# Kernel tuning notes

Measured on AMD Instinct MI355X. Metric: run time of the kernel, lower is better.

## Reference

```python
import jax, jax.numpy as jnp
import numpy as np

BATCH, SEQ, D_MODEL = 2, 2048, 1024
NUM_HEADS = 16
D_K = D_MODEL // NUM_HEADS  # 64
ROPE_THETA = 10000.0


def setup_inputs() -> dict:
    key = jax.random.key(0)
    ks = jax.random.split(key, 5)
    sigma = np.sqrt(2.0 / (D_MODEL + D_MODEL))
    return {
        "x": jax.random.normal(ks[0], (BATCH, SEQ, D_MODEL), dtype=jnp.float32),
        "Wq": jax.random.normal(ks[1], (D_MODEL, D_MODEL), dtype=jnp.float32) * sigma,
        "Wk": jax.random.normal(ks[2], (D_MODEL, D_MODEL), dtype=jnp.float32) * sigma,
        "Wv": jax.random.normal(ks[3], (D_MODEL, D_MODEL), dtype=jnp.float32) * sigma,
        "Wo": jax.random.normal(ks[4], (D_MODEL, D_MODEL), dtype=jnp.float32) * sigma,
        "token_positions": jnp.arange(SEQ, dtype=jnp.int32),
    }


def _rope(t, cos, sin):
    # t: [b, h, s, d_k]; cos/sin: [s, d_k//2]
    even, odd = t[..., ::2], t[..., 1::2]
    out_even = even * cos - odd * sin
    out_odd = odd * cos + even * sin
    return jnp.stack([out_even, out_odd], axis=-1).reshape(t.shape)


def reference(x, Wq, Wk, Wv, Wo, token_positions):
    b, s, d = x.shape
    h, dk = NUM_HEADS, D_K

    def split_heads(w):
        # Linear: einsum('... d_in, d_out d_in -> ... d_out')
        y = jnp.einsum('bsd,ed->bse', x, w)
        return y.reshape(b, s, h, dk).transpose(0, 2, 1, 3)  # [b,h,s,dk]

    q, k, v = split_heads(Wq), split_heads(Wk), split_heads(Wv)

    # RoPE tables from token positions
    inv_freq = 1.0 / (ROPE_THETA ** (jnp.arange(0, dk, 2, dtype=jnp.float32) / dk))
    freqs = token_positions.astype(jnp.float32)[:, None] * inv_freq[None, :]  # [s, dk/2]
    cos, sin = jnp.cos(freqs), jnp.sin(freqs)
    q = _rope(q, cos, sin)
    k = _rope(k, cos, sin)

    scale = 1.0 / jnp.sqrt(jnp.asarray(dk, dtype=x.dtype))
    scores = jnp.einsum('bhqd,bhkd->bhqk', q, k) * scale  # [b,h,s,s]
    causal = jnp.tril(jnp.ones((s, s), dtype=bool))
    scores = jnp.where(causal, scores, -jnp.inf)
    probs = jax.nn.softmax(scores, axis=-1)
    out = jnp.einsum('bhqk,bhkd->bhqd', probs, v)
    out = out.transpose(0, 2, 1, 3).reshape(b, s, d)
    return jnp.einsum('bsd,ed->bse', out, Wo)
```

## Files before the change

kernel.cpp:

```cpp
#include <hip/hip_runtime.h>
#include <hip/hip_bf16.h>


#define BATCH   2
#define SEQLEN  2048
#define DMODEL  1024
#define NHEADS  16
#define DK      64

typedef __attribute__((ext_vector_type(8))) short bf16x8;
typedef __attribute__((ext_vector_type(4))) short bf16x4;
typedef __attribute__((ext_vector_type(4))) float f32x4;

__device__ __forceinline__ void gload_lds16(const void* g, void* l) {
  __builtin_amdgcn_global_load_lds(
      (const __attribute__((address_space(1))) unsigned int*)g,
      (__attribute__((address_space(3))) unsigned int*)l, 16, 0, 0);
}

__device__ __forceinline__ float fast_exp2(float x) {
#if __has_builtin(__builtin_amdgcn_exp2f)
  return __builtin_amdgcn_exp2f(x);
#else
  return exp2f(x);
#endif
}

__global__ __launch_bounds__(256) void cast_all(
    const float* __restrict__ x,  const float* __restrict__ wq,
    const float* __restrict__ wk, const float* __restrict__ wv,
    const float* __restrict__ wo,
    __hip_bfloat16* __restrict__ xb,  __hip_bfloat16* __restrict__ wqb,
    __hip_bfloat16* __restrict__ wkb, __hip_bfloat16* __restrict__ wvb,
    __hip_bfloat16* __restrict__ wob) {
  const size_t MM = (size_t)1 << 20;
  size_t i = ((size_t)blockIdx.x * 256 + threadIdx.x) * 8;
  const float* src; __hip_bfloat16* dst; size_t off = i;
  if (i < 4 * MM)      { src = x;  dst = xb; }
  else if (i < 5 * MM) { src = wq; dst = wqb; off = i - 4 * MM; }
  else if (i < 6 * MM) { src = wk; dst = wkb; off = i - 5 * MM; }
  else if (i < 7 * MM) { src = wv; dst = wvb; off = i - 6 * MM; }
  else                 { src = wo; dst = wob; off = i - 7 * MM; }
  float4 a = *(const float4*)(src + off);
  float4 b = *(const float4*)(src + off + 4);
  __hip_bfloat16 t[8];
  t[0] = __float2bfloat16(a.x); t[1] = __float2bfloat16(a.y);
  t[2] = __float2bfloat16(a.z); t[3] = __float2bfloat16(a.w);
  t[4] = __float2bfloat16(b.x); t[5] = __float2bfloat16(b.y);
  t[6] = __float2bfloat16(b.z); t[7] = __float2bfloat16(b.w);
  *(bf16x8*)(dst + off) = *(const bf16x8*)t;
}

__device__ __forceinline__ void gemm_core(
    const __hip_bfloat16* __restrict__ A, const __hip_bfloat16* __restrict__ W,
    int bm, int bn, int K, f32x4 (&acc)[4][4]) {
  __shared__ __hip_bfloat16 As[128 * 32];
  __shared__ __hip_bfloat16 Ws[128 * 32];
  const int tid  = threadIdx.x;
  const int wave = tid >> 6, lane = tid & 63;
  const int col  = lane & 15, quad = lane >> 4;
  const int wm   = (wave & 1) * 64, wn = (wave >> 1) * 64;
  const int srow = wave * 32;
  const int l4   = lane >> 2, sl = lane & 3;

  for (int k0 = 0; k0 < K; k0 += 32) {
#pragma unroll
    for (int c = 0; c < 2; ++c) {
      int r = srow + c * 16 + l4;
      int g = sl ^ (r & 3);
      gload_lds16(A + (size_t)(bm + r) * K + k0 + g * 8, &As[(srow + c * 16) * 32]);
      gload_lds16(W + (size_t)(bn + r) * K + k0 + g * 8, &Ws[(srow + c * 16) * 32]);
    }
    __syncthreads();
    bf16x8 af[4], bfr[4];
#pragma unroll
    for (int mt = 0; mt < 4; ++mt) {
      int r = wm + mt * 16 + col;
      af[mt] = *(const bf16x8*)&As[r * 32 + ((quad ^ (r & 3)) * 8)];
    }
#pragma unroll
    for (int nt = 0; nt < 4; ++nt) {
      int r = wn + nt * 16 + col;
      bfr[nt] = *(const bf16x8*)&Ws[r * 32 + ((quad ^ (r & 3)) * 8)];
    }
#pragma unroll
    for (int mt = 0; mt < 4; ++mt)
#pragma unroll
      for (int nt = 0; nt < 4; ++nt)
        acc[mt][nt] = __builtin_amdgcn_mfma_f32_16x16x32_bf16(af[mt], bfr[nt], acc[mt][nt], 0, 0, 0);
    __syncthreads();
  }
}

__global__ __launch_bounds__(256) void mfma_qkv(
    const __hip_bfloat16* __restrict__ xb,
    const __hip_bfloat16* __restrict__ wqb,
    const __hip_bfloat16* __restrict__ wkb,
    const __hip_bfloat16* __restrict__ wvb,
    __hip_bfloat16* __restrict__ Qw,
    __hip_bfloat16* __restrict__ Kw,
    __hip_bfloat16* __restrict__ Vtw) {
  const int z = blockIdx.z;
  const __hip_bfloat16* W = (z == 0) ? wqb : (z == 1) ? wkb : wvb;
  const int bm = blockIdx.x * 128, bn = blockIdx.y * 128;
  f32x4 acc[4][4] = {};
  gemm_core(xb, W, bm, bn, DMODEL, acc);

  const int wave = threadIdx.x >> 6, lane = threadIdx.x & 63;
  const int col  = lane & 15, quad = lane >> 4;
  const int wm   = (wave & 1) * 64, wn = (wave >> 1) * 64;

  if (z < 2) {
    __hip_bfloat16* C = (z == 0) ? Qw : Kw;
#pragma unroll
    for (int mt = 0; mt < 4; ++mt)
#pragma unroll
      for (int nt = 0; nt < 4; ++nt) {
        int n = bn + wn + nt * 16 + col;
#pragma unroll
        for (int r = 0; r < 4; ++r) {
          int m = bm + wm + mt * 16 + quad * 4 + r;
          C[(size_t)m * DMODEL + n] = __float2bfloat16(acc[mt][nt][r]);
        }
      }
  } else {
#pragma unroll
    for (int mt = 0; mt < 4; ++mt)
#pragma unroll
      for (int nt = 0; nt < 4; ++nt) {
        int n  = bn + wn + nt * 16 + col;
        int m0 = bm + wm + mt * 16 + quad * 4;
        __hip_bfloat16 t[4];
#pragma unroll
        for (int r = 0; r < 4; ++r) t[r] = __float2bfloat16(acc[mt][nt][r]);
        size_t off = (((size_t)(m0 >> 11) * NHEADS + (n >> 6)) * DK + (n & 63)) * SEQLEN + (m0 & 2047);
        *(bf16x4*)(Vtw + off) = *(const bf16x4*)t;
      }
  }
}

__global__ __launch_bounds__(256) void mfma_out(
    const __hip_bfloat16* __restrict__ Ow,
    const __hip_bfloat16* __restrict__ wob,
    float* __restrict__ out) {
  const int bm = blockIdx.x * 128, bn = blockIdx.y * 128;
  f32x4 acc[4][4] = {};
  gemm_core(Ow, wob, bm, bn, DMODEL, acc);
  const int wave = threadIdx.x >> 6, lane = threadIdx.x & 63;
  const int col  = lane & 15, quad = lane >> 4;
  const int wm   = (wave & 1) * 64, wn = (wave >> 1) * 64;
#pragma unroll
  for (int mt = 0; mt < 4; ++mt)
#pragma unroll
    for (int nt = 0; nt < 4; ++nt) {
      int n = bn + wn + nt * 16 + col;
#pragma unroll
      for (int r = 0; r < 4; ++r) {
        int m = bm + wm + mt * 16 + quad * 4 + r;
        out[(size_t)m * DMODEL + n] = acc[mt][nt][r];
      }
    }
}

__global__ __launch_bounds__(256) void rope_kernel(
    __hip_bfloat16* __restrict__ Q,
    __hip_bfloat16* __restrict__ Kt,
    const int* __restrict__ pos, int npairs) {
  int idx = blockIdx.x * blockDim.x + threadIdx.x;
  if (idx >= npairs) return;
  int ip = idx & 511;
  int s  = (idx >> 9) & (SEQLEN - 1);
  int p  = ip & 31;
  float inv_freq = exp2f(-13.287712379549449f * ((float)(2 * p) / 64.0f));
  float ang = (float)pos[s] * inv_freq;
  float sn, cs;
  sincosf(ang, &sn, &cs);
  const float SCL = 0.18033688011112042f;
  size_t off = (size_t)idx * 2;
  float qe = __bfloat162float(Q[off]), qo = __bfloat162float(Q[off + 1]);
  Q[off]     = __float2bfloat16((qe * cs - qo * sn) * SCL);
  Q[off + 1] = __float2bfloat16((qo * cs + qe * sn) * SCL);
  float ke = __bfloat162float(Kt[off]), ko = __bfloat162float(Kt[off + 1]);
  Kt[off]     = __float2bfloat16(ke * cs - ko * sn);
  Kt[off + 1] = __float2bfloat16(ko * cs + ke * sn);
}

__global__ __launch_bounds__(256) void attn_mfma(
    const __hip_bfloat16* __restrict__ Q,
    const __hip_bfloat16* __restrict__ K,
    const __hip_bfloat16* __restrict__ Vt,
    __hip_bfloat16* __restrict__ O) {
  __shared__ __align__(16) __hip_bfloat16 Ks[2][64 * 64];
  __shared__ __align__(16) __hip_bfloat16 Vs[2][64 * 64];
  __shared__ __align__(16) __hip_bfloat16 Pl[4][16 * 64];
  const int bh = blockIdx.y;
  const int b = bh >> 4, h = bh & 15;
  const int strip = 31 - (int)blockIdx.x;
  const int wave = threadIdx.x >> 6;
  const int lane = threadIdx.x & 63;
  const int col = lane & 15;
  const int quad = lane >> 4;
  const int q0 = strip * 64 + wave * 16;
  const int cswz = col & 7;

  const size_t qkbase = ((size_t)b * SEQLEN) * DMODEL + (size_t)h * DK;
  const size_t vbase  = (size_t)bh * DK * SEQLEN;
  __hip_bfloat16* pl = &Pl[wave][0];

  const int srow = lane >> 3;
  const int slot = lane & 7;

  auto stage = [&](int t, int buf) {
    const int j0 = t * 64;
#pragma unroll
    for (int c = 0; c < 2; ++c) {
      const int r = wave * 16 + c * 8 + srow;
      const int g = slot ^ (r & 7);
      gload_lds16(K + qkbase + (size_t)(j0 + r) * DMODEL + g * 8,
                  &Ks[buf][(wave * 16 + c * 8) * 64]);
      gload_lds16(Vt + vbase + (size_t)r * SEQLEN + j0 + g * 8,
                  &Vs[buf][(wave * 16 + c * 8) * 64]);
    }
  };

  bf16x8 qf[2];
#pragma unroll
  for (int kc = 0; kc < 2; ++kc)
    qf[kc] = *(const bf16x8*)(Q + qkbase + (size_t)(q0 + col) * DMODEL + kc * 32 + quad * 8);

  f32x4 acc[4] = {};
  float m_i = -1e30f, l_i = 0.f;
  const int ntiles = strip + 1;

  stage(0, 0);
  __syncthreads();

  for (int t = 0; t < ntiles; ++t) {
    const int buf = t & 1;
    if (t + 1 < ntiles) stage(t + 1, buf ^ 1);
    const int j0 = t * 64;

    f32x4 s[4] = {};
#pragma unroll
    for (int kt = 0; kt < 4; ++kt) {
      const int row = kt * 16 + col;
#pragma unroll
      for (int kc = 0; kc < 2; ++kc) {
        bf16x8 kf = *(const bf16x8*)&Ks[buf][row * 64 + (((kc * 4 + quad) ^ cswz) * 8)];
        s[kt] = __builtin_amdgcn_mfma_f32_16x16x32_bf16(kf, qf[kc], s[kt], 0, 0, 0);
      }
    }

    if (t == strip) {
      const int q = q0 + col;
#pragma unroll
      for (int kt = 0; kt < 4; ++kt)
#pragma unroll
        for (int r = 0; r < 4; ++r)
          if (j0 + kt * 16 + quad * 4 + r > q) s[kt][r] = -1e30f;
    }

    float mx = m_i;
#pragma unroll
    for (int kt = 0; kt < 4; ++kt)
#pragma unroll
      for (int r = 0; r < 4; ++r) mx = fmaxf(mx, s[kt][r]);
    mx = fmaxf(mx, __shfl_xor(mx, 16, 64));
    mx = fmaxf(mx, __shfl_xor(mx, 32, 64));
    float alpha = fast_exp2(m_i - mx);
    m_i = mx;

    float rs = 0.f;
#pragma unroll
    for (int kt = 0; kt < 4; ++kt) {
      __hip_bfloat16 tp[4];
#pragma unroll
      for (int r = 0; r < 4; ++r) {
        float pv = fast_exp2(s[kt][r] - mx);
        rs += pv;
        tp[r] = __float2bfloat16(pv);
      }
      int c = ((kt << 1) | (quad >> 1)) ^ cswz;
      *(bf16x4*)(pl + col * 64 + c * 8 + (quad & 1) * 4) = *(const bf16x4*)tp;
    }
    rs += __shfl_xor(rs, 16, 64);
    rs += __shfl_xor(rs, 32, 64);
    l_i = l_i * alpha + rs;
#pragma unroll
    for (int dt = 0; dt < 4; ++dt) acc[dt] *= alpha;

#pragma unroll
    for (int jc = 0; jc < 2; ++jc) {
      int c = ((jc << 2) | quad) ^ cswz;
      bf16x8 pf = *(const bf16x8*)(pl + col * 64 + c * 8);
#pragma unroll
      for (int dt = 0; dt < 4; ++dt) {
        const int dv = dt * 16 + col;
        bf16x8 vf = *(const bf16x8*)&Vs[buf][dv * 64 + (((jc * 4 + quad) ^ cswz) * 8)];
        acc[dt] = __builtin_amdgcn_mfma_f32_16x16x32_bf16(vf, pf, acc[dt], 0, 0, 0);
      }
    }

    __syncthreads();
  }

  const float inv = 1.f / l_i;
  const size_t orow = qkbase + (size_t)(q0 + col) * DMODEL;
#pragma unroll
  for (int dt = 0; dt < 4; ++dt) {
    __hip_bfloat16 tp[4];
#pragma unroll
    for (int r = 0; r < 4; ++r) tp[r] = __float2bfloat16(acc[dt][r] * inv);
    *(bf16x4*)(O + orow + dt * 16 + quad * 4) = *(const bf16x4*)tp;
  }
}

extern "C" void kernel_launch(void* const* d_in, const int* in_sizes, int n_in,
                              void* d_out, int out_size, void* d_ws, size_t ws_size,
                              hipStream_t stream) {
  const float* x  = (const float*)d_in[0];
  const float* Wq = (const float*)d_in[1];
  const float* Wk = (const float*)d_in[2];
  const float* Wv = (const float*)d_in[3];
  const float* Wo = (const float*)d_in[4];
  const int* pos  = (const int*)d_in[5];
  float* out = (float*)d_out;

  const size_t NELEM = (size_t)BATCH * SEQLEN * DMODEL;
  const size_t WELEM = (size_t)DMODEL * DMODEL;
  __hip_bfloat16* xb  = (__hip_bfloat16*)d_ws;
  __hip_bfloat16* Qw  = xb + NELEM;
  __hip_bfloat16* Kw  = Qw + NELEM;
  __hip_bfloat16* Vtw = Kw + NELEM;
  __hip_bfloat16* wqb = Vtw + NELEM;
  __hip_bfloat16* wkb = wqb + WELEM;
  __hip_bfloat16* wvb = wkb + WELEM;
  __hip_bfloat16* wob = wvb + WELEM;
  __hip_bfloat16* Ow  = xb;

  cast_all<<<4096, 256, 0, stream>>>(x, Wq, Wk, Wv, Wo, xb, wqb, wkb, wvb, wob);

  mfma_qkv<<<dim3(32, 8, 3), 256, 0, stream>>>(xb, wqb, wkb, wvb, Qw, Kw, Vtw);

  int npairs = BATCH * SEQLEN * (DMODEL / 2);
  rope_kernel<<<(npairs + 255) / 256, 256, 0, stream>>>(Qw, Kw, pos, npairs);

  attn_mfma<<<dim3(32, BATCH * NHEADS), 256, 0, stream>>>(Qw, Kw, Vtw, Ow);

  mfma_out<<<dim3(32, 8), 256, 0, stream>>>(Ow, wob, out);
}
```

Baseline: 214.8 us.

## Fuse RoPE into QKV epilogue and widen attention blocks to 128 query rows

RoPE and the Q scaling are now applied inside the QKV GEMM epilogue, with a lane shuffle supplying the pair partner, so the separate rope kernel and its extra global read/write pass over Q and K go away. The attention kernel now gives each wave 32 query rows (two 16-row tiles), which reuses each K/V LDS fragment across two MFMAs. Blocks are remapped so each XCD works on a fixed set of heads, and waves skip key tiles beyond their causal limit. In exchange, the epilogue recomputes sincos per element, and the attention kernel uses more registers and LDS, which may reduce occupancy.

```diff
diff --git a/kernel.cpp b/kernel.cpp
--- a/kernel.cpp
+++ b/kernel.cpp
@@ -97,6 +97,7 @@
     const __hip_bfloat16* __restrict__ wqb,
     const __hip_bfloat16* __restrict__ wkb,
     const __hip_bfloat16* __restrict__ wvb,
+    const int* __restrict__ pos,
     __hip_bfloat16* __restrict__ Qw,
     __hip_bfloat16* __restrict__ Kw,
     __hip_bfloat16* __restrict__ Vtw) {
@@ -112,15 +113,26 @@
 
   if (z < 2) {
     __hip_bfloat16* C = (z == 0) ? Qw : Kw;
+    const float SCLQ = 0.18033688011112042f;
+    const bool odd = col & 1;
 #pragma unroll
     for (int mt = 0; mt < 4; ++mt)
 #pragma unroll
       for (int nt = 0; nt < 4; ++nt) {
         int n = bn + wn + nt * 16 + col;
+        int p = (n & 63) >> 1;
+        float invf = exp2f((float)p * -0.4152410118609203f);
 #pragma unroll
         for (int r = 0; r < 4; ++r) {
           int m = bm + wm + mt * 16 + quad * 4 + r;
-          C[(size_t)m * DMODEL + n] = __float2bfloat16(acc[mt][nt][r]);
+          float ang = (float)pos[m & (SEQLEN - 1)] * invf;
+          float sn, cs;
+          sincosf(ang, &sn, &cs);
+          float v  = acc[mt][nt][r];
+          float pv = __shfl_xor(v, 1, 64);
+          float res = odd ? (v * cs + pv * sn) : (v * cs - pv * sn);
+          if (z == 0) res *= SCLQ;
+          C[(size_t)m * DMODEL + n] = __float2bfloat16(res);
         }
       }
   } else {
@@ -162,29 +174,6 @@
     }
 }
 
-__global__ __launch_bounds__(256) void rope_kernel(
-    __hip_bfloat16* __restrict__ Q,
-    __hip_bfloat16* __restrict__ Kt,
-    const int* __restrict__ pos, int npairs) {
-  int idx = blockIdx.x * blockDim.x + threadIdx.x;
-  if (idx >= npairs) return;
-  int ip = idx & 511;
-  int s  = (idx >> 9) & (SEQLEN - 1);
-  int p  = ip & 31;
-  float inv_freq = exp2f(-13.287712379549449f * ((float)(2 * p) / 64.0f));
-  float ang = (float)pos[s] * inv_freq;
-  float sn, cs;
-  sincosf(ang, &sn, &cs);
-  const float SCL = 0.18033688011112042f;
-  size_t off = (size_t)idx * 2;
-  float qe = __bfloat162float(Q[off]), qo = __bfloat162float(Q[off + 1]);
-  Q[off]     = __float2bfloat16((qe * cs - qo * sn) * SCL);
-  Q[off + 1] = __float2bfloat16((qo * cs + qe * sn) * SCL);
-  float ke = __bfloat162float(Kt[off]), ko = __bfloat162float(Kt[off + 1]);
-  Kt[off]     = __float2bfloat16(ke * cs - ko * sn);
-  Kt[off + 1] = __float2bfloat16(ko * cs + ke * sn);
-}
-
 __global__ __launch_bounds__(256) void attn_mfma(
     const __hip_bfloat16* __restrict__ Q,
     const __hip_bfloat16* __restrict__ K,
@@ -192,15 +181,17 @@
     __hip_bfloat16* __restrict__ O) {
   __shared__ __align__(16) __hip_bfloat16 Ks[2][64 * 64];
   __shared__ __align__(16) __hip_bfloat16 Vs[2][64 * 64];
-  __shared__ __align__(16) __hip_bfloat16 Pl[4][16 * 64];
-  const int bh = blockIdx.y;
+  __shared__ __align__(16) __hip_bfloat16 Pl[4][32 * 64];
+  const int lin  = (int)blockIdx.y * (int)gridDim.x + (int)blockIdx.x;
+  const int xcd  = lin & 7, slot = lin >> 3;
+  const int bh   = xcd * 4 + (slot & 3);
+  const int strip = 15 - (slot >> 2);
   const int b = bh >> 4, h = bh & 15;
-  const int strip = 31 - (int)blockIdx.x;
   const int wave = threadIdx.x >> 6;
   const int lane = threadIdx.x & 63;
   const int col = lane & 15;
   const int quad = lane >> 4;
-  const int q0 = strip * 64 + wave * 16;
+  const int q0w = strip * 128 + wave * 32;
   const int cswz = col & 7;
 
   const size_t qkbase = ((size_t)b * SEQLEN) * DMODEL + (size_t)h * DK;
@@ -208,14 +199,14 @@
   __hip_bfloat16* pl = &Pl[wave][0];
 
   const int srow = lane >> 3;
-  const int slot = lane & 7;
+  const int slot16 = lane & 7;
 
   auto stage = [&](int t, int buf) {
     const int j0 = t * 64;
 #pragma unroll
     for (int c = 0; c < 2; ++c) {
       const int r = wave * 16 + c * 8 + srow;
-      const int g = slot ^ (r & 7);
+      const int g = slot16 ^ (r & 7);
       gload_lds16(K + qkbase + (size_t)(j0 + r) * DMODEL + g * 8,
                   &Ks[buf][(wave * 16 + c * 8) * 64]);
       gload_lds16(Vt + vbase + (size_t)r * SEQLEN + j0 + g * 8,
@@ -223,14 +214,19 @@
     }
   };
 
-  bf16x8 qf[2];
-#pragma unroll
-  for (int kc = 0; kc < 2; ++kc)
-    qf[kc] = *(const bf16x8*)(Q + qkbase + (size_t)(q0 + col) * DMODEL + kc * 32 + quad * 8);
-
-  f32x4 acc[4] = {};
-  float m_i = -1e30f, l_i = 0.f;
-  const int ntiles = strip + 1;
+  bf16x8 qf[2][2];
+#pragma unroll
+  for (int qt = 0; qt < 2; ++qt)
+#pragma unroll
+    for (int kc = 0; kc < 2; ++kc)
+      qf[qt][kc] = *(const bf16x8*)(Q + qkbase +
+          (size_t)(q0w + qt * 16 + col) * DMODEL + kc * 32 + quad * 8);
+
+  f32x4 acc[2][4] = {};
+  float m_i[2] = {-1e30f, -1e30f}, l_i[2] = {0.f, 0.f};
+
+  const int ntiles = 2 * strip + 2;
+  const int tl_w   = 2 * strip + (wave >> 1);
 
   stage(0, 0);
   __syncthreads();
@@ -238,80 +234,100 @@
   for (int t = 0; t < ntiles; ++t) {
     const int buf = t & 1;
     if (t + 1 < ntiles) stage(t + 1, buf ^ 1);
-    const int j0 = t * 64;
-
-    f32x4 s[4] = {};
-#pragma unroll
-    for (int kt = 0; kt < 4; ++kt) {
-      const int row = kt * 16 + col;
-#pragma unroll
-      for (int kc = 0; kc < 2; ++kc) {
-        bf16x8 kf = *(const bf16x8*)&Ks[buf][row * 64 + (((kc * 4 + quad) ^ cswz) * 8)];
-        s[kt] = __builtin_amdgcn_mfma_f32_16x16x32_bf16(kf, qf[kc], s[kt], 0, 0, 0);
-      }
-    }
-
-    if (t == strip) {
-      const int q = q0 + col;
-#pragma unroll
-      for (int kt = 0; kt < 4; ++kt)
-#pragma unroll
-        for (int r = 0; r < 4; ++r)
-          if (j0 + kt * 16 + quad * 4 + r > q) s[kt][r] = -1e30f;
-    }
-
-    float mx = m_i;
-#pragma unroll
-    for (int kt = 0; kt < 4; ++kt)
-#pragma unroll
-      for (int r = 0; r < 4; ++r) mx = fmaxf(mx, s[kt][r]);
-    mx = fmaxf(mx, __shfl_xor(mx, 16, 64));
-    mx = fmaxf(mx, __shfl_xor(mx, 32, 64));
-    float alpha = fast_exp2(m_i - mx);
-    m_i = mx;
-
-    float rs = 0.f;
-#pragma unroll
-    for (int kt = 0; kt < 4; ++kt) {
-      __hip_bfloat16 tp[4];
-#pragma unroll
-      for (int r = 0; r < 4; ++r) {
-        float pv = fast_exp2(s[kt][r] - mx);
-        rs += pv;
-        tp[r] = __float2bfloat16(pv);
-      }
-      int c = ((kt << 1) | (quad >> 1)) ^ cswz;
-      *(bf16x4*)(pl + col * 64 + c * 8 + (quad & 1) * 4) = *(const bf16x4*)tp;
-    }
-    rs += __shfl_xor(rs, 16, 64);
-    rs += __shfl_xor(rs, 32, 64);
-    l_i = l_i * alpha + rs;
-#pragma unroll
-    for (int dt = 0; dt < 4; ++dt) acc[dt] *= alpha;
-
-#pragma unroll
-    for (int jc = 0; jc < 2; ++jc) {
-      int c = ((jc << 2) | quad) ^ cswz;
-      bf16x8 pf = *(const bf16x8*)(pl + col * 64 + c * 8);
-#pragma unroll
-      for (int dt = 0; dt < 4; ++dt) {
-        const int dv = dt * 16 + col;
-        bf16x8 vf = *(const bf16x8*)&Vs[buf][dv * 64 + (((jc * 4 + quad) ^ cswz) * 8)];
-        acc[dt] = __builtin_amdgcn_mfma_f32_16x16x32_bf16(vf, pf, acc[dt], 0, 0, 0);
+
+    if (t <= tl_w) {
+      const int j0 = t * 64;
+
+      f32x4 s[2][4] = {};
+#pragma unroll
+      for (int kt = 0; kt < 4; ++kt) {
+        const int row = kt * 16 + col;
+#pragma unroll
+        for (int kc = 0; kc < 2; ++kc) {
+          bf16x8 kf = *(const bf16x8*)&Ks[buf][row * 64 + (((kc * 4 + quad) ^ cswz) * 8)];
+#pragma unroll
+          for (int qt = 0; qt < 2; ++qt)
+            s[qt][kt] = __builtin_amdgcn_mfma_f32_16x16x32_bf16(kf, qf[qt][kc], s[qt][kt], 0, 0, 0);
+        }
+      }
+
+      if (t == tl_w) {
+#pragma unroll
+        for (int qt = 0; qt < 2; ++qt) {
+          const int q = q0w + qt * 16 + col;
+#pragma unroll
+          for (int kt = 0; kt < 4; ++kt)
+#pragma unroll
+            for (int r = 0; r < 4; ++r)
+              if (j0 + kt * 16 + quad * 4 + r > q) s[qt][kt][r] = -1e30f;
+        }
+      }
+
+#pragma unroll
+      for (int qt = 0; qt < 2; ++qt) {
+        float mx = m_i[qt];
+#pragma unroll
+        for (int kt = 0; kt < 4; ++kt)
+#pragma unroll
+          for (int r = 0; r < 4; ++r) mx = fmaxf(mx, s[qt][kt][r]);
+        mx = fmaxf(mx, __shfl_xor(mx, 16, 64));
+        mx = fmaxf(mx, __shfl_xor(mx, 32, 64));
+        float alpha = fast_exp2(m_i[qt] - mx);
+        m_i[qt] = mx;
+
+        float rs = 0.f;
+#pragma unroll
+        for (int kt = 0; kt < 4; ++kt) {
+          __hip_bfloat16 tp[4];
+#pragma unroll
+          for (int r = 0; r < 4; ++r) {
+            float pv = fast_exp2(s[qt][kt][r] - mx);
+            rs += pv;
+            tp[r] = __float2bfloat16(pv);
+          }
+          int c = ((kt << 1) | (quad >> 1)) ^ cswz;
+          *(bf16x4*)(pl + (qt * 16 + col) * 64 + c * 8 + (quad & 1) * 4) = *(const bf16x4*)tp;
+        }
+        rs += __shfl_xor(rs, 16, 64);
+        rs += __shfl_xor(rs, 32, 64);
+        l_i[qt] = l_i[qt] * alpha + rs;
+#pragma unroll
+        for (int dt = 0; dt < 4; ++dt) acc[qt][dt] *= alpha;
+      }
+
+#pragma unroll
+      for (int jc = 0; jc < 2; ++jc) {
+        bf16x8 pf[2];
+#pragma unroll
+        for (int qt = 0; qt < 2; ++qt) {
+          int c = ((jc << 2) | quad) ^ cswz;
+          pf[qt] = *(const bf16x8*)(pl + (qt * 16 + col) * 64 + c * 8);
+        }
+#pragma unroll
+        for (int dt = 0; dt < 4; ++dt) {
+          const int dv = dt * 16 + col;
+          bf16x8 vf = *(const bf16x8*)&Vs[buf][dv * 64 + (((jc * 4 + quad) ^ cswz) * 8)];
+#pragma unroll
+          for (int qt = 0; qt < 2; ++qt)
+            acc[qt][dt] = __builtin_amdgcn_mfma_f32_16x16x32_bf16(vf, pf[qt], acc[qt][dt], 0, 0, 0);
+        }
       }
     }
 
     __syncthreads();
   }
 
-  const float inv = 1.f / l_i;
-  const size_t orow = qkbase + (size_t)(q0 + col) * DMODEL;
-#pragma unroll
-  for (int dt = 0; dt < 4; ++dt) {
-    __hip_bfloat16 tp[4];
-#pragma unroll
-    for (int r = 0; r < 4; ++r) tp[r] = __float2bfloat16(acc[dt][r] * inv);
-    *(bf16x4*)(O + orow + dt * 16 + quad * 4) = *(const bf16x4*)tp;
+#pragma unroll
+  for (int qt = 0; qt < 2; ++qt) {
+    const float inv = 1.f / l_i[qt];
+    const size_t orow = qkbase + (size_t)(q0w + qt * 16 + col) * DMODEL;
+#pragma unroll
+    for (int dt = 0; dt < 4; ++dt) {
+      __hip_bfloat16 tp[4];
+#pragma unroll
+      for (int r = 0; r < 4; ++r) tp[r] = __float2bfloat16(acc[qt][dt][r] * inv);
+      *(bf16x4*)(O + orow + dt * 16 + quad * 4) = *(const bf16x4*)tp;
+    }
   }
 }
 
@@ -340,12 +356,9 @@
 
   cast_all<<<4096, 256, 0, stream>>>(x, Wq, Wk, Wv, Wo, xb, wqb, wkb, wvb, wob);
 
-  mfma_qkv<<<dim3(32, 8, 3), 256, 0, stream>>>(xb, wqb, wkb, wvb, Qw, Kw, Vtw);
-
-  int npairs = BATCH * SEQLEN * (DMODEL / 2);
-  rope_kernel<<<(npairs + 255) / 256, 256, 0, stream>>>(Qw, Kw, pos, npairs);
-
-  attn_mfma<<<dim3(32, BATCH * NHEADS), 256, 0, stream>>>(Qw, Kw, Vtw, Ow);
+  mfma_qkv<<<dim3(32, 8, 3), 256, 0, stream>>>(xb, wqb, wkb, wvb, pos, Qw, Kw, Vtw);
+
+  attn_mfma<<<dim3(16, BATCH * NHEADS), 256, 0, stream>>>(Qw, Kw, Vtw, Ow);
 
   mfma_out<<<dim3(32, 8), 256, 0, stream>>>(Ow, wob, out);
 }
```

Result: slower. 657.5 us (+206.1%).
